# Kernel tuning notes

Hardware: AMD Instinct MI355X
Metric: run time of the kernel (lower is better)

## Reference

```python
import jax, jax.numpy as jnp
from jax import lax
import numpy as np

B, S, D, H, O, V = 1024, 128, 256, 2048, 10, 10

def setup_inputs() -> dict:
    key = jax.random.key(0)
    ks = jax.random.split(key, 8)
    x = jax.random.randint(ks[0], (B, S), 0, V)
    embed = jax.random.normal(ks[1], (V, D), dtype=jnp.float32)
    sd_hx = 1.0 / np.sqrt(D)
    sd_hh = 1.0 / np.sqrt(H)
    W_hx = jax.random.uniform(ks[2], (H, D), minval=-sd_hx, maxval=sd_hx)
    b_hx = jax.random.uniform(ks[3], (H,), minval=-sd_hx, maxval=sd_hx)
    W_hh = jax.random.uniform(ks[4], (H, H), minval=-sd_hh, maxval=sd_hh)
    b_hh = jax.random.uniform(ks[5], (H,), minval=-sd_hh, maxval=sd_hh)
    W_oh = jax.random.uniform(ks[6], (O, H), minval=-sd_hh, maxval=sd_hh)
    b_oh = jax.random.uniform(ks[7], (O,), minval=-sd_hh, maxval=sd_hh)
    return {"x": x, "embed": embed, "W_hx": W_hx, "b_hx": b_hx,
            "W_hh": W_hh, "b_hh": b_hh, "W_oh": W_oh, "b_oh": b_oh}

def reference(x, embed, W_hx, b_hx, W_hh, b_hh, W_oh, b_oh):
    e = embed[x]                                   # [B,S,D]
    # precompute input-to-hidden projection for all steps (one big GEMM)
    xh = jnp.einsum('bsd,hd->bsh', e, W_hx) + b_hx  # [B,S,H]
    # step 0: torch code applies ONLY hx (no hh term, no hh bias)
    h0 = jnp.tanh(xh[:, 0])
    def step(h, xt):
        h = jnp.tanh(xt + h @ W_hh.T + b_hh)
        return h, None
    hT, _ = lax.scan(step, h0, jnp.swapaxes(xh[:, 1:], 0, 1))  # scan over time
    o = hT @ W_oh.T + b_oh                         # [B,O]
    return jax.nn.softmax(o, axis=1)               # nn.Softmax() on 2D -> dim=1
```

## Files before the change

kernel.cpp:

```cpp
#include <hip/hip_runtime.h>
#include <stdint.h>
#include <stddef.h>

#define B_ 1024
#define S_ 128
#define D_ 256
#define H_ 2048
#define O_ 10
#define V_ 10

#define BM 64
#define BN 64
#define BK 128
#define NKT (H_ / BK)

typedef unsigned short u16;
typedef short v8s __attribute__((ext_vector_type(8)));
typedef float v4f __attribute__((ext_vector_type(4)));
typedef u16 u16x4 __attribute__((ext_vector_type(4)));

__device__ __forceinline__ u16 f2bf(float f) {
  unsigned int u = __float_as_uint(f);
  u += 0x7FFFu + ((u >> 16) & 1u);
  return (u16)(u >> 16);
}
__device__ __forceinline__ float bf2f(u16 h) {
  return __uint_as_float(((unsigned int)h) << 16);
}
__device__ __forceinline__ float fast_tanh(float x) {
  float e = __expf(2.0f * x);
  return 1.0f - 2.0f / (e + 1.0f);
}
__device__ __forceinline__ void gl2lds16(const void* g, void* l) {
  __builtin_amdgcn_global_load_lds(
      (const __attribute__((address_space(1))) uint32_t*)g,
      (__attribute__((address_space(3))) uint32_t*)l, 16, 0, 0);
}

__global__ __launch_bounds__(256) void make_table(const float* __restrict__ embed,
                                                  const float* __restrict__ W_hx,
                                                  const float* __restrict__ b_hx,
                                                  float* __restrict__ Txh) {
  int idx = blockIdx.x * 256 + threadIdx.x;
  int v = idx >> 11, h = idx & 2047;
  const float4* e4 = (const float4*)(embed + v * D_);
  const float4* w4 = (const float4*)(W_hx + (size_t)h * D_);
  float s = b_hx[h];
#pragma unroll 4
  for (int d = 0; d < D_ / 4; ++d) {
    float4 a = e4[d], b = w4[d];
    s = fmaf(a.x, b.x, s); s = fmaf(a.y, b.y, s);
    s = fmaf(a.z, b.z, s); s = fmaf(a.w, b.w, s);
  }
  Txh[idx] = s;
}

__global__ __launch_bounds__(256) void conv_w(const float* __restrict__ W,
                                              u16* __restrict__ Wb) {
  int i = blockIdx.x * 256 + threadIdx.x;
  float4 w = ((const float4*)W)[i];
  u16x4 o = { f2bf(w.x), f2bf(w.y), f2bf(w.z), f2bf(w.w) };
  ((u16x4*)Wb)[i] = o;
}

__global__ __launch_bounds__(256) void init_h0(const float* __restrict__ Txh,
                                               const int* __restrict__ x,
                                               u16* __restrict__ H0) {
  int idx = blockIdx.x * 256 + threadIdx.x;
  int b = idx >> 11, j = idx & 2047;
  int xv = x[b * S_];
  H0[idx] = f2bf(fast_tanh(Txh[xv * H_ + j]));
}


__device__ __forceinline__ void stage_tiles(const u16* __restrict__ Hin,
                                            const u16* __restrict__ Wb,
                                            u16* __restrict__ As, u16* __restrict__ Bs,
                                            int bm, int bn, int kbase, int tid, int w) {
#pragma unroll
  for (int i = 0; i < 4; ++i) {
    int s = i * 256 + tid;
    int m = s >> 4;
    int cg = (s & 15) ^ (m & 15);
    const u16* g = Hin + (size_t)(bm + m) * H_ + kbase + cg * 8;
    u16* lp = As + (size_t)(i * 256 + (w << 6)) * 8;
    gl2lds16(g, lp);
  }
#pragma unroll
  for (int i = 0; i < 4; ++i) {
    int s = i * 256 + tid;
    int n = s >> 4;
    int cg = (s & 15) ^ (n & 15);
    const u16* g = Wb + (size_t)(bn + n) * H_ + kbase + cg * 8;
    u16* lp = Bs + (size_t)(i * 256 + (w << 6)) * 8;
    gl2lds16(g, lp);
  }
}

__global__ __launch_bounds__(256, 2) void rnn_step(const u16* __restrict__ Hin,
                                                   const u16* __restrict__ Wb,
                                                   const float* __restrict__ Txh,
                                                   const int* __restrict__ x,
                                                   const float* __restrict__ b_hh,
                                                   u16* __restrict__ Hout,
                                                   int t) {
  __shared__ __align__(16) u16 As[2][BM * BK];
  __shared__ __align__(16) u16 Bs[2][BN * BK];

  const int tid = threadIdx.x;
  const int bid = blockIdx.x;
  const int xcd = bid & 7;
  const int sl = bid >> 3;
  const int bn = (xcd * 4 + (sl & 3)) * BN;
  const int bm = (sl >> 2) * BM;

  const int w = tid >> 6, l = tid & 63;
  const int wr = w >> 1, wc = w & 1;
  const int lane16 = l & 15, quad = l >> 4;

  v4f acc[2][2];
#pragma unroll
  for (int i = 0; i < 2; ++i)
#pragma unroll
    for (int j = 0; j < 2; ++j) acc[i][j] = (v4f){0.f, 0.f, 0.f, 0.f};

  stage_tiles(Hin, Wb, As[0], Bs[0], bm, bn, 0, tid, w);
  __syncthreads();

  for (int kt = 0; kt < NKT; ++kt) {
    const int cur = kt & 1;
    if (kt + 1 < NKT)
      stage_tiles(Hin, Wb, As[cur ^ 1], Bs[cur ^ 1], bm, bn, (kt + 1) * BK, tid, w);

#pragma unroll
    for (int kc = 0; kc < 4; ++kc) {
      const int cc = kc * 4 + quad;
      v8s a[2], bf[2];
#pragma unroll
      for (int i = 0; i < 2; ++i) {
        int m = wr * 32 + i * 16 + lane16;
        a[i] = *(const v8s*)&As[cur][(m * 16 + (cc ^ lane16)) * 8];
      }
#pragma unroll
      for (int j = 0; j < 2; ++j) {
        int n = wc * 32 + j * 16 + lane16;
        bf[j] = *(const v8s*)&Bs[cur][(n * 16 + (cc ^ lane16)) * 8];
      }
#pragma unroll
      for (int i = 0; i < 2; ++i)
#pragma unroll
        for (int j = 0; j < 2; ++j)
          acc[i][j] = __builtin_amdgcn_mfma_f32_16x16x32_bf16(a[i], bf[j], acc[i][j], 0, 0, 0);
    }
    __syncthreads();
  }

  const int colb = bn + wc * 32 + lane16;
  float bh[2];
#pragma unroll
  for (int j = 0; j < 2; ++j) bh[j] = b_hh[colb + j * 16];
#pragma unroll
  for (int i = 0; i < 2; ++i) {
#pragma unroll
    for (int r = 0; r < 4; ++r) {
      int row = bm + wr * 32 + i * 16 + quad * 4 + r;
      const float* trow = Txh + x[row * S_ + t] * H_;
      u16* orow = Hout + (size_t)row * H_;
#pragma unroll
      for (int j = 0; j < 2; ++j) {
        int col = colb + j * 16;
        float v = acc[i][j][r] + trow[col] + bh[j];
        orow[col] = f2bf(fast_tanh(v));
      }
    }
  }
}

__global__ __launch_bounds__(256) void out_softmax(const u16* __restrict__ Hf,
                                                   const float* __restrict__ W_oh,
                                                   const float* __restrict__ b_oh,
                                                   float* __restrict__ out) {
  int b = blockIdx.x, tid = threadIdx.x;
  float hv[8];
  const u16* hr = Hf + (size_t)b * H_ + tid * 8;
#pragma unroll
  for (int u = 0; u < 8; ++u) hv[u] = bf2f(hr[u]);
  float acc[O_];
#pragma unroll
  for (int i = 0; i < O_; ++i) {
    const float* wr = W_oh + (size_t)i * H_ + tid * 8;
    float s = 0.f;
#pragma unroll
    for (int u = 0; u < 8; ++u) s = fmaf(hv[u], wr[u], s);
    acc[i] = s;
  }
#pragma unroll
  for (int off = 32; off > 0; off >>= 1)
#pragma unroll
    for (int i = 0; i < O_; ++i) acc[i] += __shfl_down(acc[i], off);
  __shared__ float red[4][O_];
  if ((tid & 63) == 0)
#pragma unroll
    for (int i = 0; i < O_; ++i) red[tid >> 6][i] = acc[i];
  __syncthreads();
  if (tid == 0) {
    float o[O_], mx = -1e30f;
#pragma unroll
    for (int i = 0; i < O_; ++i) {
      o[i] = red[0][i] + red[1][i] + red[2][i] + red[3][i] + b_oh[i];
      mx = fmaxf(mx, o[i]);
    }
    float se = 0.f;
#pragma unroll
    for (int i = 0; i < O_; ++i) { o[i] = __expf(o[i] - mx); se += o[i]; }
    float inv = 1.f / se;
#pragma unroll
    for (int i = 0; i < O_; ++i) out[b * O_ + i] = o[i] * inv;
  }
}

extern "C" void kernel_launch(void* const* d_in, const int* in_sizes, int n_in,
                              void* d_out, int out_size, void* d_ws, size_t ws_size,
                              hipStream_t stream) {
  const int*   x     = (const int*)  d_in[0];
  const float* embed = (const float*)d_in[1];
  const float* W_hx  = (const float*)d_in[2];
  const float* b_hx  = (const float*)d_in[3];
  const float* W_hh  = (const float*)d_in[4];
  const float* b_hh  = (const float*)d_in[5];
  const float* W_oh  = (const float*)d_in[6];
  const float* b_oh  = (const float*)d_in[7];
  float* out = (float*)d_out;

  char* ws = (char*)d_ws;
  float* Txh = (float*)ws;
  u16* Wb = (u16*)(ws + (80 << 10));
  u16* Ha = (u16*)(ws + (80 << 10) + (8 << 20));
  u16* Hb = (u16*)(ws + (80 << 10) + (12 << 20));

  make_table<<<80, 256, 0, stream>>>(embed, W_hx, b_hx, Txh);
  conv_w<<<4096, 256, 0, stream>>>(W_hh, Wb);
  init_h0<<<8192, 256, 0, stream>>>(Txh, x, Ha);

  for (int t = 1; t < S_; ++t) {
    const u16* hin = (t & 1) ? Ha : Hb;
    u16* hout = (t & 1) ? Hb : Ha;
    rnn_step<<<512, 256, 0, stream>>>(hin, Wb, Txh, x, b_hh, hout, t);
  }
  out_softmax<<<B_, 256, 0, stream>>>(Hb, W_oh, b_oh, out);
}
```

Measured before the change: 2.352 ms.

## Replace per-step launches with persistent kernel keeping W_hh slice resident in LDS

The 127 separate rnn_step launches become one persistent kernel of 256 blocks. Each block loads a 32-column slice of bf16 W_hh (128 KB) into LDS once and reuses it for every timestep. Hidden-state rows are streamed from global memory straight into registers with double buffering. Steps are separated by a two-level atomic grid barrier (per-XCD counters, then a global flag), which removes launch overhead and repeated weight reloads. The cost is that all 256 blocks must be co-resident, the hidden state must be exchanged through L2/global memory across XCDs, and the spin loop's timeout can break the barrier and race on the hidden state.

```diff
diff --git a/kernel.cpp b/kernel.cpp
--- a/kernel.cpp
+++ b/kernel.cpp
@@ -9,11 +9,6 @@
 #define O_ 10
 #define V_ 10
 
-#define BM 64
-#define BN 64
-#define BK 128
-#define NKT (H_ / BK)
-
 typedef unsigned short u16;
 typedef short v8s __attribute__((ext_vector_type(8)));
 typedef float v4f __attribute__((ext_vector_type(4)));
@@ -35,6 +30,10 @@
   __builtin_amdgcn_global_load_lds(
       (const __attribute__((address_space(1))) uint32_t*)g,
       (__attribute__((address_space(3))) uint32_t*)l, 16, 0, 0);
+}
+
+__global__ void zero_sync(int* __restrict__ sync) {
+  sync[threadIdx.x] = 0;
 }
 
 __global__ __launch_bounds__(256) void make_table(const float* __restrict__ embed,
@@ -72,107 +71,128 @@
   H0[idx] = f2bf(fast_tanh(Txh[xv * H_ + j]));
 }
 
-
-__device__ __forceinline__ void stage_tiles(const u16* __restrict__ Hin,
-                                            const u16* __restrict__ Wb,
-                                            u16* __restrict__ As, u16* __restrict__ Bs,
-                                            int bm, int bn, int kbase, int tid, int w) {
-#pragma unroll
-  for (int i = 0; i < 4; ++i) {
-    int s = i * 256 + tid;
-    int m = s >> 4;
-    int cg = (s & 15) ^ (m & 15);
-    const u16* g = Hin + (size_t)(bm + m) * H_ + kbase + cg * 8;
-    u16* lp = As + (size_t)(i * 256 + (w << 6)) * 8;
-    gl2lds16(g, lp);
-  }
-#pragma unroll
-  for (int i = 0; i < 4; ++i) {
-    int s = i * 256 + tid;
-    int n = s >> 4;
-    int cg = (s & 15) ^ (n & 15);
-    const u16* g = Wb + (size_t)(bn + n) * H_ + kbase + cg * 8;
-    u16* lp = Bs + (size_t)(i * 256 + (w << 6)) * 8;
-    gl2lds16(g, lp);
-  }
-}
-
-__global__ __launch_bounds__(256, 2) void rnn_step(const u16* __restrict__ Hin,
-                                                   const u16* __restrict__ Wb,
-                                                   const float* __restrict__ Txh,
-                                                   const int* __restrict__ x,
-                                                   const float* __restrict__ b_hh,
-                                                   u16* __restrict__ Hout,
-                                                   int t) {
-  __shared__ __align__(16) u16 As[2][BM * BK];
-  __shared__ __align__(16) u16 Bs[2][BN * BK];
+__global__ __launch_bounds__(512, 2) void rnn_persist(u16* __restrict__ Ha,
+                                                      u16* __restrict__ Hb,
+                                                      const u16* __restrict__ Wb,
+                                                      const float* __restrict__ Txh,
+                                                      const int* __restrict__ x,
+                                                      const float* __restrict__ b_hh,
+                                                      int* sync) {
+  __shared__ __align__(16) u16 Wlds[32 * 2048];
 
   const int tid = threadIdx.x;
   const int bid = blockIdx.x;
-  const int xcd = bid & 7;
-  const int sl = bid >> 3;
-  const int bn = (xcd * 4 + (sl & 3)) * BN;
-  const int bm = (sl >> 2) * BM;
+  const int mg = (bid >> 1) & 3;
+  const int ng = ((bid >> 3) << 1) | (bid & 1);
+  const int mbase = mg * 256;
+  const int nbase = ng * 32;
 
   const int w = tid >> 6, l = tid & 63;
-  const int wr = w >> 1, wc = w & 1;
   const int lane16 = l & 15, quad = l >> 4;
 
-  v4f acc[2][2];
-#pragma unroll
-  for (int i = 0; i < 2; ++i)
-#pragma unroll
-    for (int j = 0; j < 2; ++j) acc[i][j] = (v4f){0.f, 0.f, 0.f, 0.f};
-
-  stage_tiles(Hin, Wb, As[0], Bs[0], bm, bn, 0, tid, w);
+#pragma unroll
+  for (int it = 0; it < 16; ++it) {
+    int s = it * 512 + tid;
+    int n = s >> 8, cs = s & 255;
+    int c = cs ^ (n & 15);
+    const u16* g = Wb + (size_t)(nbase + n) * H_ + c * 8;
+    u16* lp = Wlds + (size_t)(it * 512 + (w << 6)) * 8;
+    gl2lds16(g, lp);
+  }
   __syncthreads();
 
-  for (int kt = 0; kt < NKT; ++kt) {
-    const int cur = kt & 1;
-    if (kt + 1 < NKT)
-      stage_tiles(Hin, Wb, As[cur ^ 1], Bs[cur ^ 1], bm, bn, (kt + 1) * BK, tid, w);
-
-#pragma unroll
-    for (int kc = 0; kc < 4; ++kc) {
-      const int cc = kc * 4 + quad;
-      v8s a[2], bf[2];
-#pragma unroll
-      for (int i = 0; i < 2; ++i) {
-        int m = wr * 32 + i * 16 + lane16;
-        a[i] = *(const v8s*)&As[cur][(m * 16 + (cc ^ lane16)) * 8];
-      }
-#pragma unroll
-      for (int j = 0; j < 2; ++j) {
-        int n = wc * 32 + j * 16 + lane16;
-        bf[j] = *(const v8s*)&Bs[cur][(n * 16 + (cc ^ lane16)) * 8];
-      }
-#pragma unroll
-      for (int i = 0; i < 2; ++i)
-#pragma unroll
-        for (int j = 0; j < 2; ++j)
-          acc[i][j] = __builtin_amdgcn_mfma_f32_16x16x32_bf16(a[i], bf[j], acc[i][j], 0, 0, 0);
-    }
+  const int mstrip = mbase + w * 32;
+
+  for (int t = 1; t < S_; ++t) {
+    const u16* Hin = (t & 1) ? Ha : Hb;
+    u16* Hout = (t & 1) ? Hb : Ha;
+
+    v4f acc[2][2];
+#pragma unroll
+    for (int i = 0; i < 2; ++i)
+#pragma unroll
+      for (int j = 0; j < 2; ++j) acc[i][j] = (v4f){0.f, 0.f, 0.f, 0.f};
+
+    const u16* ar0 = Hin + (size_t)(mstrip + lane16) * H_ + quad * 8;
+    const u16* ar1 = Hin + (size_t)(mstrip + 16 + lane16) * H_ + quad * 8;
+
+    v8s abuf[2][2][4];
+#pragma unroll
+    for (int c = 0; c < 4; ++c) {
+      abuf[0][0][c] = *(const v8s*)(ar0 + c * 32);
+      abuf[0][1][c] = *(const v8s*)(ar1 + c * 32);
+    }
+
+#pragma unroll 4
+    for (int g = 0; g < 16; ++g) {
+      const int par = g & 1, nxt = par ^ 1;
+      if (g < 15) {
+#pragma unroll
+        for (int c = 0; c < 4; ++c) {
+          int off = ((g + 1) * 4 + c) * 32;
+          abuf[nxt][0][c] = *(const v8s*)(ar0 + off);
+          abuf[nxt][1][c] = *(const v8s*)(ar1 + off);
+        }
+      }
+#pragma unroll
+      for (int c = 0; c < 4; ++c) {
+        int c8 = (g * 4 + c) * 4 + quad;
+        v8s bf[2];
+#pragma unroll
+        for (int j = 0; j < 2; ++j) {
+          int n = j * 16 + lane16;
+          int cs = c8 ^ (n & 15);
+          bf[j] = *(const v8s*)&Wlds[((size_t)n * 256 + cs) * 8];
+        }
+#pragma unroll
+        for (int i = 0; i < 2; ++i)
+#pragma unroll
+          for (int j = 0; j < 2; ++j)
+            acc[i][j] = __builtin_amdgcn_mfma_f32_16x16x32_bf16(abuf[par][i][c], bf[j],
+                                                                acc[i][j], 0, 0, 0);
+      }
+    }
+
+    const int colb = nbase + lane16;
+    float bh[2];
+#pragma unroll
+    for (int j = 0; j < 2; ++j) bh[j] = b_hh[colb + j * 16];
+#pragma unroll
+    for (int i = 0; i < 2; ++i) {
+#pragma unroll
+      for (int r = 0; r < 4; ++r) {
+        int row = mstrip + i * 16 + quad * 4 + r;
+        const float* trow = Txh + x[row * S_ + t] * H_;
+        u16* orow = Hout + (size_t)row * H_;
+#pragma unroll
+        for (int j = 0; j < 2; ++j) {
+          int col = colb + j * 16;
+          float v = acc[i][j][r] + trow[col] + bh[j];
+          orow[col] = f2bf(fast_tanh(v));
+        }
+      }
+    }
+
     __syncthreads();
-  }
-
-  const int colb = bn + wc * 32 + lane16;
-  float bh[2];
-#pragma unroll
-  for (int j = 0; j < 2; ++j) bh[j] = b_hh[colb + j * 16];
-#pragma unroll
-  for (int i = 0; i < 2; ++i) {
-#pragma unroll
-    for (int r = 0; r < 4; ++r) {
-      int row = bm + wr * 32 + i * 16 + quad * 4 + r;
-      const float* trow = Txh + x[row * S_ + t] * H_;
-      u16* orow = Hout + (size_t)row * H_;
-#pragma unroll
-      for (int j = 0; j < 2; ++j) {
-        int col = colb + j * 16;
-        float v = acc[i][j][r] + trow[col] + bh[j];
-        orow[col] = f2bf(fast_tanh(v));
-      }
-    }
+    if (tid == 0) {
+      __builtin_amdgcn_fence(__ATOMIC_RELEASE, "");
+      int a = __hip_atomic_fetch_add(&sync[(bid & 7) * 32], 1,
+                                     __ATOMIC_RELAXED, __HIP_MEMORY_SCOPE_AGENT);
+      if (a == t * 32 - 1) {
+        int b = __hip_atomic_fetch_add(&sync[256], 1,
+                                       __ATOMIC_RELAXED, __HIP_MEMORY_SCOPE_AGENT);
+        if (b == t * 8 - 1)
+          __hip_atomic_store(&sync[288], t, __ATOMIC_RELEASE, __HIP_MEMORY_SCOPE_AGENT);
+      }
+      int spin = 0;
+      while (__hip_atomic_load(&sync[288], __ATOMIC_RELAXED,
+                               __HIP_MEMORY_SCOPE_AGENT) < t) {
+        __builtin_amdgcn_s_sleep(8);
+        if (++spin > (1 << 22)) break;
+      }
+    }
+    __syncthreads();
+    __builtin_amdgcn_fence(__ATOMIC_ACQUIRE, "");
   }
 }
 
@@ -234,18 +254,17 @@
 
   char* ws = (char*)d_ws;
   float* Txh = (float*)ws;
-  u16* Wb = (u16*)(ws + (80 << 10));
-  u16* Ha = (u16*)(ws + (80 << 10) + (8 << 20));
-  u16* Hb = (u16*)(ws + (80 << 10) + (12 << 20));
-
+  u16* Wb    = (u16*)(ws + (80 << 10));
+  u16* Ha    = (u16*)(ws + (80 << 10) + (8 << 20));
+  u16* Hb    = (u16*)(ws + (80 << 10) + (12 << 20));
+  int* syncp = (int*)(ws + (80 << 10) + (16 << 20));
+
+  zero_sync<<<1, 512, 0, stream>>>(syncp);
   make_table<<<80, 256, 0, stream>>>(embed, W_hx, b_hx, Txh);
   conv_w<<<4096, 256, 0, stream>>>(W_hh, Wb);
   init_h0<<<8192, 256, 0, stream>>>(Txh, x, Ha);
 
-  for (int t = 1; t < S_; ++t) {
-    const u16* hin = (t & 1) ? Ha : Hb;
-    u16* hout = (t & 1) ? Hb : Ha;
-    rnn_step<<<512, 256, 0, stream>>>(hin, Wb, Txh, x, b_hh, hout, t);
-  }
+  rnn_persist<<<256, 512, 0, stream>>>(Ha, Hb, Wb, Txh, x, b_hh, syncp);
+
   out_softmax<<<B_, 256, 0, stream>>>(Hb, W_oh, b_oh, out);
 }
```

Result: slower. 7.125 ms (+202.9%).
